# Kernel tuning notes

Hardware: AMD Instinct MI355X
Metric: run time of the kernel (lower is better)

Reference implementation:

```python
import jax, jax.numpy as jnp
import numpy as np

V_TH = 1.0
LENS, SCALE, HIGHT, GAMMA = 0.5, 6.0, 0.15, 0.5  # MultiGaussian surrogate constants (DH-SNN)


def _gauss(x, mu, sigma):
    return jnp.exp(-((x - mu) ** 2) / (2.0 * sigma ** 2)) / (jnp.sqrt(2.0 * jnp.pi) * sigma)


@jax.custom_vjp
def spike_fn(x):
    return (x > 0).astype(x.dtype)


def _spike_fwd(x):
    return spike_fn(x), x


def _spike_bwd(x, g):
    sg = GAMMA * (_gauss(x, 0.0, LENS) * (1.0 + HIGHT)
                  - _gauss(x, LENS, SCALE * LENS) * HIGHT
                  - _gauss(x, -LENS, SCALE * LENS) * HIGHT)
    return (g * sg,)


spike_fn.defvjp(_spike_fwd, _spike_bwd)


def setup_inputs() -> dict:
    key = jax.random.key(0)
    ks = jax.random.split(key, 12)
    B, T, I, H, O = 128, 784, 512, 512, 10
    xavier_in = lambda k, sh: jax.random.normal(k, sh, jnp.float32) * jnp.sqrt(2.0 / (sh[0] + sh[1]))
    return {
        'input_data': jax.random.normal(ks[0], (B, T, I), jnp.float32),
        'W1': xavier_in(ks[1], (H, I)),
        'b1': jnp.zeros((H,), jnp.float32),
        'W2': xavier_in(ks[2], (H, I)),
        'b2': jnp.zeros((H,), jnp.float32),
        'tau_m': jax.random.uniform(ks[3], (H,), jnp.float32, 0.0, 4.0),
        'tau_n1': jax.random.uniform(ks[4], (H,), jnp.float32, 2.0, 6.0),
        'tau_n2': jax.random.uniform(ks[5], (H,), jnp.float32, -4.0, 0.0),
        'Wr': xavier_in(ks[6], (O, H)),
        'br': jnp.zeros((O,), jnp.float32),
        'mem0': jax.random.uniform(ks[7], (B, H), jnp.float32),
        'spike0': jax.random.uniform(ks[8], (B, H), jnp.float32),
    }


def reference(input_data, W1, b1, W2, b2, tau_m, tau_n1, tau_n2, Wr, br, mem0, spike0):
    # Batched branch projections for all timesteps (big GEMMs, done once)
    d1_all = jnp.einsum('bti,hi->bth', input_data, W1) + b1  # [B,T,H]
    d2_all = jnp.einsum('bti,hi->bth', input_data, W2) + b2

    alpha = jax.nn.sigmoid(tau_m)    # membrane decay
    beta1 = jax.nn.sigmoid(tau_n1)   # branch-1 dendritic decay
    beta2 = jax.nn.sigmoid(tau_n2)   # branch-2 dendritic decay

    B, H = mem0.shape
    d1_init = jnp.zeros((B, H), input_data.dtype)
    d2_init = jnp.zeros((B, H), input_data.dtype)

    def step(carry, xs):
        mem, spk, d1, d2 = carry
        d1_t, d2_t = xs
        d1 = beta1 * d1 + (1.0 - beta1) * d1_t
        d2 = beta2 * d2 + (1.0 - beta2) * d2_t
        total = d1 + d2
        mem = mem * alpha + (1.0 - alpha) * total - V_TH * spk
        spk = spike_fn(mem - V_TH)
        return (mem, spk, d1, d2), spk

    xs = (jnp.swapaxes(d1_all, 0, 1), jnp.swapaxes(d2_all, 0, 1))  # [T,B,H]
    _, spikes = jax.lax.scan(step, (mem0, spike0, d1_init, d2_init), xs)
    spikes = jnp.swapaxes(spikes, 0, 1)  # [B,T,H]
    out = jnp.einsum('bth,oh->bto', spikes, Wr) + br  # readout per timestep
    return out
```

## Files before the change

### kernel.cpp

```cpp
#include <hip/hip_runtime.h>
#include <cmath>

#define HD 512
#define IN 512
#define TT 784
#define BB 128
#define MH 50176

typedef short short8 __attribute__((ext_vector_type(8)));
typedef unsigned short ushort8 __attribute__((ext_vector_type(8)));
typedef float floatx4 __attribute__((ext_vector_type(4)));

#define GLDS(gp, lp) __builtin_amdgcn_global_load_lds( \
    (const __attribute__((address_space(1))) void*)(gp), \
    (__attribute__((address_space(3))) void*)(lp), 16, 0, 0)

__device__ __forceinline__ unsigned short bf16_rne(float x) {
    unsigned u = __float_as_uint(x);
    unsigned r = u + 0x7FFFu + ((u >> 16) & 1u);
    return (unsigned short)(r >> 16);
}
__device__ __forceinline__ float bf16_f(unsigned short s) {
    return __uint_as_float(((unsigned)s) << 16);
}

__global__ __launch_bounds__(256) void split3(
    const float* __restrict__ src, unsigned short* __restrict__ p1,
    unsigned short* __restrict__ p2, unsigned short* __restrict__ p3, long n8)
{
    long g = (long)blockIdx.x * 256 + threadIdx.x;
    if (g >= n8) return;
    const float* xp = src + g * 8;
    ushort8 o1, o2, o3;
#pragma unroll
    for (int j = 0; j < 8; ++j) {
        float x = xp[j];
        unsigned short s1 = bf16_rne(x);
        float r1 = x - bf16_f(s1);
        unsigned short s2 = bf16_rne(r1);
        float r2 = r1 - bf16_f(s2);
        unsigned short s3 = bf16_rne(r2);
        o1[j] = s1; o2[j] = s2; o3[j] = s3;
    }
    *(ushort8*)(p1 + g * 8) = o1;
    *(ushort8*)(p2 + g * 8) = o2;
    *(ushort8*)(p3 + g * 8) = o3;
}

__global__ __launch_bounds__(256, 2) void gemm_bf16x3(
    const unsigned short* __restrict__ Xp,
    const unsigned short* __restrict__ Wp,
    const float* __restrict__ b1, const float* __restrict__ b2,
    float* __restrict__ d1buf, float* __restrict__ d2buf)
{
    __shared__ unsigned short lds[6][128][32];
    unsigned short* lflat = &lds[0][0][0];
    const int tid  = threadIdx.x;
    const int lane = tid & 63;
    const int w    = tid >> 6;
    const int pn = blockIdx.x & 7;
    const int pm = blockIdx.x >> 3;
    const int m0 = pm * 128;
    const int n0 = pn * 128;

    const unsigned short* gp[12];
    {
        const int rsub = lane >> 2;
        const int csub = (lane & 3) * 8;
#pragma unroll
        for (int j = 0; j < 12; ++j) {
            int seg = w * 12 + j;
            int p = seg >> 3, sub = seg & 7;
            int row16 = sub * 16 + rsub;
            gp[j] = (p < 3)
              ? Xp + ((size_t)p * MH + m0 + row16) * IN + csub
              : Wp + ((size_t)(p - 3) * 1024 + n0 + row16) * IN + csub;
        }
    }

    floatx4 acc[4][4];
#pragma unroll
    for (int i = 0; i < 4; ++i)
#pragma unroll
        for (int j = 0; j < 4; ++j) acc[i][j] = (floatx4){0.f, 0.f, 0.f, 0.f};

    const int wm = w >> 1, wn = w & 1;
    const int c16 = lane & 15;
    const int q8  = (lane >> 4) * 8;

    for (int ks = 0; ks < IN; ks += 32) {
#pragma unroll
        for (int j = 0; j < 12; ++j)
            GLDS(gp[j] + ks, lflat + (size_t)(w * 12 + j) * 512);
        __syncthreads();

        short8 Bf[3][4];
#pragma unroll
        for (int p = 0; p < 3; ++p)
#pragma unroll
            for (int fj = 0; fj < 4; ++fj)
                Bf[p][fj] = *(const short8*)&lds[3 + p][wn * 64 + fj * 16 + c16][q8];

#pragma unroll
        for (int fi = 0; fi < 4; ++fi) {
            const int r = wm * 64 + fi * 16 + c16;
            short8 a1 = *(const short8*)&lds[0][r][q8];
            short8 a2 = *(const short8*)&lds[1][r][q8];
            short8 a3 = *(const short8*)&lds[2][r][q8];
#pragma unroll
            for (int fj = 0; fj < 4; ++fj) {
                floatx4 c = acc[fi][fj];
                c = __builtin_amdgcn_mfma_f32_16x16x32_bf16(a3, Bf[0][fj], c, 0, 0, 0);
                c = __builtin_amdgcn_mfma_f32_16x16x32_bf16(a2, Bf[1][fj], c, 0, 0, 0);
                c = __builtin_amdgcn_mfma_f32_16x16x32_bf16(a1, Bf[2][fj], c, 0, 0, 0);
                c = __builtin_amdgcn_mfma_f32_16x16x32_bf16(a2, Bf[0][fj], c, 0, 0, 0);
                c = __builtin_amdgcn_mfma_f32_16x16x32_bf16(a1, Bf[1][fj], c, 0, 0, 0);
                c = __builtin_amdgcn_mfma_f32_16x16x32_bf16(a1, Bf[0][fj], c, 0, 0, 0);
                acc[fi][fj] = c;
            }
        }
        __syncthreads();
    }

    const int quad = lane >> 4;
    const bool first = (n0 < HD);
    const float* bias = first ? b1 : b2;
    float* obuf = first ? d1buf : d2buf;
    const int nb = n0 & (HD - 1);
    float bv[4];
#pragma unroll
    for (int fj = 0; fj < 4; ++fj) bv[fj] = bias[nb + wn * 64 + fj * 16 + c16];
#pragma unroll
    for (int fi = 0; fi < 4; ++fi) {
#pragma unroll
        for (int fj = 0; fj < 4; ++fj) {
            int n = nb + wn * 64 + fj * 16 + c16;
#pragma unroll
            for (int r = 0; r < 4; ++r) {
                int m = m0 + wm * 64 + fi * 16 + quad * 4 + r;
                obuf[(size_t)m * HD + n] = acc[fi][fj][r] + bv[fj];
            }
        }
    }
}

__global__ __launch_bounds__(64) void scan_half(
    const float* __restrict__ d1buf, const float* __restrict__ d2buf,
    const float* __restrict__ tau_m, const float* __restrict__ tau_n1,
    const float* __restrict__ tau_n2,
    const float* __restrict__ mem0, const float* __restrict__ spike0,
    unsigned short* __restrict__ spikes, int b0)
{
    const int gid = blockIdx.x * 64 + threadIdx.x;
    const int h  = gid & (HD - 1);
    const int bl = gid >> 9;
    const int b  = b0 + bl;
    const float alpha = 1.f / (1.f + expf(-tau_m[h]));
    const float be1   = 1.f / (1.f + expf(-tau_n1[h]));
    const float be2   = 1.f / (1.f + expf(-tau_n2[h]));
    float mem = mem0[b * HD + h];
    float spk = spike0[b * HD + h];
    float d1 = 0.f, d2 = 0.f;
    const float* p1 = d1buf + (size_t)bl * TT * HD + h;
    const float* p2 = d2buf + (size_t)bl * TT * HD + h;
    unsigned short* sp = spikes + (size_t)b * (TT / 16) * HD + h;

#pragma unroll 1
    for (int g = 0; g < TT / 16; ++g) {
        float a1[16], a2[16];
#pragma unroll
        for (int i = 0; i < 16; ++i) {
            a1[i] = p1[(size_t)(g * 16 + i) * HD];
            a2[i] = p2[(size_t)(g * 16 + i) * HD];
        }
        unsigned int word = 0;
#pragma unroll
        for (int i = 0; i < 16; ++i) {
            d1 = be1 * d1 + (1.f - be1) * a1[i];
            d2 = be2 * d2 + (1.f - be2) * a2[i];
            float total = d1 + d2;
            mem = mem * alpha + (1.f - alpha) * total - spk;
            bool fire = (mem - 1.0f) > 0.f;
            spk = fire ? 1.f : 0.f;
            word |= (fire ? 1u : 0u) << i;
        }
        sp[(size_t)g * HD] = (unsigned short)word;
    }
}

__global__ __launch_bounds__(256) void readout(
    const unsigned short* __restrict__ spikes,
    const float* __restrict__ Wr, const float* __restrict__ br,
    float* __restrict__ out)
{
    __shared__ float WrS[10 * HD];
    __shared__ float brS[10];
    const int tid = threadIdx.x;
    for (int i = tid; i < 10 * HD; i += 256) WrS[i] = Wr[i];
    if (tid < 10) brS[tid] = br[tid];
    __syncthreads();

    const int gid = blockIdx.x * 256 + tid;
    const int t = gid % TT;
    const int b = gid / TT;
    const int tw  = t >> 4;
    const int bit = t & 15;
    const unsigned short* row = spikes + ((size_t)b * (TT / 16) + tw) * HD;

    float acc[10];
#pragma unroll
    for (int o = 0; o < 10; ++o) acc[o] = brS[o];

    for (int h = 0; h < HD; ++h) {
        float s = (float)((row[h] >> bit) & 1);
#pragma unroll
        for (int o = 0; o < 10; ++o) acc[o] = fmaf(s, WrS[o * HD + h], acc[o]);
    }
    float* op = out + (size_t)gid * 10;
#pragma unroll
    for (int o = 0; o < 10; ++o) op[o] = acc[o];
}

extern "C" void kernel_launch(void* const* d_in, const int* in_sizes, int n_in,
                              void* d_out, int out_size, void* d_ws, size_t ws_size,
                              hipStream_t stream)
{
    const float* X      = (const float*)d_in[0];
    const float* W1     = (const float*)d_in[1];
    const float* b1     = (const float*)d_in[2];
    const float* W2     = (const float*)d_in[3];
    const float* b2     = (const float*)d_in[4];
    const float* tau_m  = (const float*)d_in[5];
    const float* tau_n1 = (const float*)d_in[6];
    const float* tau_n2 = (const float*)d_in[7];
    const float* Wr     = (const float*)d_in[8];
    const float* br     = (const float*)d_in[9];
    const float* mem0   = (const float*)d_in[10];
    const float* spike0 = (const float*)d_in[11];
    float* out = (float*)d_out;

    char* p = (char*)d_ws;
    unsigned short* Wp = (unsigned short*)p;  p += (size_t)3 * 1024 * IN * 2;
    unsigned short* Xp = (unsigned short*)p;  p += (size_t)3 * MH * IN * 2;
    float* d1buf = (float*)p;                 p += (size_t)MH * HD * 4;
    float* d2buf = (float*)p;                 p += (size_t)MH * HD * 4;
    unsigned short* spikes = (unsigned short*)p;

    const size_t WPS = (size_t)1024 * IN;
    const size_t XPS = (size_t)MH * IN;

    split3<<<dim3(128), dim3(256), 0, stream>>>(
        W1, Wp, Wp + WPS, Wp + 2 * WPS, (long)HD * IN / 8);
    split3<<<dim3(128), dim3(256), 0, stream>>>(
        W2, Wp + (size_t)HD * IN, Wp + WPS + (size_t)HD * IN,
        Wp + 2 * WPS + (size_t)HD * IN, (long)HD * IN / 8);

    for (int half = 0; half < 2; ++half) {
        split3<<<dim3((unsigned)(((long)MH * IN / 8 + 255) / 256)), dim3(256), 0, stream>>>(
            X + (size_t)half * MH * IN, Xp, Xp + XPS, Xp + 2 * XPS, (long)MH * IN / 8);
        gemm_bf16x3<<<dim3(392 * 8), dim3(256), 0, stream>>>(
            Xp, Wp, b1, b2, d1buf, d2buf);
        scan_half<<<dim3(512), dim3(64), 0, stream>>>(
            d1buf, d2buf, tau_m, tau_n1, tau_n2, mem0, spike0,
            spikes, half * 64);
    }
    readout<<<dim3(BB * TT / 256), dim3(256), 0, stream>>>(spikes, Wr, br, out);
}
```

Before: 1.116 ms.

## Remap GEMM blocks per XCD and double-buffer scan input loads

```diff
diff --git a/kernel.cpp b/kernel.cpp
--- a/kernel.cpp
+++ b/kernel.cpp
@@ -58,8 +58,10 @@
     const int tid  = threadIdx.x;
     const int lane = tid & 63;
     const int w    = tid >> 6;
-    const int pn = blockIdx.x & 7;
-    const int pm = blockIdx.x >> 3;
+    const int xcd = blockIdx.x & 7;
+    const int j   = blockIdx.x >> 3;
+    const int pm  = xcd * 49 + (j >> 3);
+    const int pn  = j & 7;
     const int m0 = pm * 128;
     const int n0 = pn * 128;
 
@@ -68,11 +70,11 @@
         const int rsub = lane >> 2;
         const int csub = (lane & 3) * 8;
 #pragma unroll
-        for (int j = 0; j < 12; ++j) {
-            int seg = w * 12 + j;
+        for (int jj = 0; jj < 12; ++jj) {
+            int seg = w * 12 + jj;
             int p = seg >> 3, sub = seg & 7;
             int row16 = sub * 16 + rsub;
-            gp[j] = (p < 3)
+            gp[jj] = (p < 3)
               ? Xp + ((size_t)p * MH + m0 + row16) * IN + csub
               : Wp + ((size_t)(p - 3) * 1024 + n0 + row16) * IN + csub;
         }
@@ -82,7 +84,7 @@
 #pragma unroll
     for (int i = 0; i < 4; ++i)
 #pragma unroll
-        for (int j = 0; j < 4; ++j) acc[i][j] = (floatx4){0.f, 0.f, 0.f, 0.f};
+        for (int jj = 0; jj < 4; ++jj) acc[i][jj] = (floatx4){0.f, 0.f, 0.f, 0.f};
 
     const int wm = w >> 1, wn = w & 1;
     const int c16 = lane & 15;
@@ -90,8 +92,8 @@
 
     for (int ks = 0; ks < IN; ks += 32) {
 #pragma unroll
-        for (int j = 0; j < 12; ++j)
-            GLDS(gp[j] + ks, lflat + (size_t)(w * 12 + j) * 512);
+        for (int jj = 0; jj < 12; ++jj)
+            GLDS(gp[jj] + ks, lflat + (size_t)(w * 12 + jj) * 512);
         __syncthreads();
 
         short8 Bf[3][4];
@@ -165,19 +167,27 @@
     const float* p2 = d2buf + (size_t)bl * TT * HD + h;
     unsigned short* sp = spikes + (size_t)b * (TT / 16) * HD + h;
 
+    float a1[2][16], a2[2][16];
+#pragma unroll
+    for (int i = 0; i < 16; ++i) {
+        a1[0][i] = p1[(size_t)i * HD];
+        a2[0][i] = p2[(size_t)i * HD];
+    }
 #pragma unroll 1
     for (int g = 0; g < TT / 16; ++g) {
-        float a1[16], a2[16];
+        const int cur = g & 1, nxt = cur ^ 1;
+        if (g + 1 < TT / 16) {
+#pragma unroll
+            for (int i = 0; i < 16; ++i) {
+                a1[nxt][i] = p1[(size_t)((g + 1) * 16 + i) * HD];
+                a2[nxt][i] = p2[(size_t)((g + 1) * 16 + i) * HD];
+            }
+        }
+        unsigned int word = 0;
 #pragma unroll
         for (int i = 0; i < 16; ++i) {
-            a1[i] = p1[(size_t)(g * 16 + i) * HD];
-            a2[i] = p2[(size_t)(g * 16 + i) * HD];
-        }
-        unsigned int word = 0;
-#pragma unroll
-        for (int i = 0; i < 16; ++i) {
-            d1 = be1 * d1 + (1.f - be1) * a1[i];
-            d2 = be2 * d2 + (1.f - be2) * a2[i];
+            d1 = be1 * d1 + (1.f - be1) * a1[cur][i];
+            d2 = be2 * d2 + (1.f - be2) * a2[cur][i];
             float total = d1 + d2;
             mem = mem * alpha + (1.f - alpha) * total - spk;
             bool fire = (mem - 1.0f) > 0.f;
```

After: 1.646 ms. 47.5% more time.
